# Kernel tuning notes

Measured on AMD Instinct MI355X. Metric: run time of the kernel, lower is better.

Reference implementation:

```python
import jax, jax.numpy as jnp
import numpy as np

NHEAD = 8


def _global_query_attention(cs, ks, vs):
    """cs: (B,H,G,Ek) global queries; ks: (B,H,S,Ek); vs: (B,H,S,Ev).
    For each key position i: v'_i = sum_{s<=i} softmax(K[:i] @ q) * V[:i].
    Returns (B,H,S,G,Ev)."""
    w = jnp.exp(jnp.einsum('bhge,bhse->bhgs', cs, ks))          # (B,H,G,S)
    norms = jnp.cumsum(w, axis=-1)                               # (B,H,G,S)
    wv = w[..., None] * vs[:, :, None, :, :]                     # (B,H,G,S,Ev) -- huge intermediate
    resp = jnp.cumsum(wv, axis=-2) / norms[..., None]            # (B,H,G,S,Ev)
    return jnp.swapaxes(resp, -3, -2)                            # (B,H,S,G,Ev)


def setup_inputs() -> dict:
    B, L, E, G = 4, 2048, 512, 16
    KD = VD = E
    keys = jax.random.split(jax.random.key(0), 9)
    s_qk = 0.02              # keep exp(q.k) finite in fp32
    s_v = 1.0 / np.sqrt(VD).astype(np.float32)
    return {
        'query':        jax.random.normal(keys[0], (B, L, E), jnp.float32),
        'key':          jax.random.normal(keys[1], (B, L, E), jnp.float32),
        'value':        jax.random.normal(keys[2], (B, L, E), jnp.float32),
        'context':      jax.random.normal(keys[3], (B, G, E), jnp.float32),
        'query_proj':   jax.random.normal(keys[4], (1, E, KD), jnp.float32) * s_qk,
        'key_proj':     jax.random.normal(keys[5], (1, E, KD), jnp.float32) * s_qk,
        'value_proj':   jax.random.normal(keys[6], (1, E, VD), jnp.float32) * s_v,
        'output_proj':  jax.random.normal(keys[7], (1, VD, E), jnp.float32) * s_v,
        'context_proj': jax.random.normal(keys[8], (1, E, KD), jnp.float32) * s_qk,
    }


def reference(query, key, value, context, query_proj, key_proj, value_proj, output_proj, context_proj):
    B, L, E = query.shape
    G = context.shape[1]
    H = NHEAD
    KD = query_proj.shape[-1]
    VD = value_proj.shape[-1]
    Ek, Ev = KD // H, VD // H

    def heads(x, W, n, dh):
        # (B,n,E) @ (1,E,D) -> (B,n,D) -> (B,H,n,dh)
        return jnp.swapaxes((x @ W).reshape(B, n, H, dh), 1, 2)

    cs = heads(context, context_proj, G, Ek)   # (B,H,G,Ek)
    qs = heads(query, query_proj, L, Ek)       # (B,H,L,Ek)
    ks = heads(key, key_proj, L, Ek)           # (B,H,S,Ek)
    vs = heads(value, value_proj, L, Ev)       # (B,H,S,Ev)

    resp_v = _global_query_attention(cs, ks, vs)   # (B,H,S,G,Ev)
    resp_k = _global_query_attention(cs, ks, ks)   # (B,H,S,G,Ek)

    logits = jnp.einsum('bhse,bhsge->bhsg', qs, resp_k)   # (B,H,S,G)
    w = jax.nn.softmax(logits, axis=-1)
    out = jnp.einsum('bhsg,bhsge->bhse', w, resp_v)       # (B,H,S,Ev)
    out = jnp.swapaxes(out, 1, 2).reshape(B, L, VD)       # (B,S,vdim)
    return out @ output_proj                               # (B,S,d_model)
```

## Files before the change

### kernel.cpp

```cpp
#include <hip/hip_runtime.h>
#include <hip/hip_bf16.h>

#define NB 4
#define SL 2048
#define NG 16
#define NH 8
#define DH 64
#define NBH (NB * NH)
#define NCH (SL / 64)

typedef __attribute__((ext_vector_type(8))) short bh8;
typedef __attribute__((ext_vector_type(4))) float fx4;

__device__ __forceinline__ ushort f2bf(float x) {
    union { float f; unsigned u; } v; v.f = x;
    const unsigned r = v.u + 0x7fffu + ((v.u >> 16) & 1u);
    return (ushort)(r >> 16);
}
__device__ __forceinline__ float b2f(ushort u) {
    union { unsigned u; float f; } v; v.u = ((unsigned)u) << 16;
    return v.f;
}
__device__ __forceinline__ bh8 pack8(float4 lo, float4 hi) {
    bh8 r;
    r[0] = (short)f2bf(lo.x); r[1] = (short)f2bf(lo.y);
    r[2] = (short)f2bf(lo.z); r[3] = (short)f2bf(lo.w);
    r[4] = (short)f2bf(hi.x); r[5] = (short)f2bf(hi.y);
    r[6] = (short)f2bf(hi.z); r[7] = (short)f2bf(hi.w);
    return r;
}
__device__ __forceinline__ void unpack8(bh8 v, float4& lo, float4& hi) {
    lo.x = b2f((ushort)v[0]); lo.y = b2f((ushort)v[1]);
    lo.z = b2f((ushort)v[2]); lo.w = b2f((ushort)v[3]);
    hi.x = b2f((ushort)v[4]); hi.y = b2f((ushort)v[5]);
    hi.z = b2f((ushort)v[6]); hi.w = b2f((ushort)v[7]);
}

__global__ __launch_bounds__(256) void convT512_4(const float* __restrict__ w0,
                                                  const float* __restrict__ w1,
                                                  const float* __restrict__ w2,
                                                  const float* __restrict__ w3,
                                                  ushort* __restrict__ o0,
                                                  ushort* __restrict__ o1,
                                                  ushort* __restrict__ o2,
                                                  ushort* __restrict__ o3) {
    const int z = blockIdx.z;
    const float* W = (z == 0) ? w0 : (z == 1) ? w1 : (z == 2) ? w2 : w3;
    ushort* WT = (z == 0) ? o0 : (z == 1) ? o1 : (z == 2) ? o2 : o3;
    __shared__ float tile[32][33];
    const int bx = blockIdx.x * 32, by = blockIdx.y * 32;
    const int tx = threadIdx.x & 31, ty = threadIdx.x >> 5;
#pragma unroll
    for (int p = 0; p < 4; ++p)
        tile[ty + p * 8][tx] = W[(size_t)(by + ty + p * 8) * 512 + bx + tx];
    __syncthreads();
#pragma unroll
    for (int p = 0; p < 4; ++p)
        WT[(size_t)(bx + ty + p * 8) * 512 + by + tx] = f2bf(tile[tx][ty + p * 8]);
}

__global__ __launch_bounds__(256, 6) void gemm_qkv_kernel(
    const float* __restrict__ qf, const float* __restrict__ kf,
    const float* __restrict__ vf, const ushort* __restrict__ qpT,
    const ushort* __restrict__ kpT, const ushort* __restrict__ vpT,
    ushort* __restrict__ qsb, ushort* __restrict__ ksb, ushort* __restrict__ vsb) {
    const int z = blockIdx.z;
    const float* A32 = (z == 0) ? qf : (z == 1) ? kf : vf;
    const ushort* BT = (z == 0) ? qpT : (z == 1) ? kpT : vpT;
    ushort* out = (z == 0) ? qsb : (z == 1) ? ksb : vsb;

    __shared__ __align__(16) ushort As[2][64 * 32];
    __shared__ __align__(16) ushort Bs[2][128 * 32];
    const int t = threadIdx.x;
    const int lane = t & 63, w = t >> 6;
    const int bm = blockIdx.x * 64, bn = blockIdx.y * 128;
    const int ea = t * 8;
    const size_t arow = (size_t)(bm + (ea >> 5)) * 512 + (ea & 31);
    const int eb0 = w * 1024 + lane * 8;
    const int eb1 = eb0 + 512;
    const size_t b0 = (size_t)(bn + (eb0 >> 5)) * 512 + (eb0 & 31);
    const size_t b1 = (size_t)(bn + (eb1 >> 5)) * 512 + (eb1 & 31);
    const int wr = w >> 1, wc = w & 1;
    const int fr = lane & 15, kg = lane >> 4;
    const int aoff = (wr * 32 + fr) * 32 + kg * 8;
    const int boff = (wc * 64 + fr) * 32 + kg * 8;
    fx4 acc[2][4] = {};
    float4 a0v, a1v;

#define LOADA(kk)                                                              \
    do {                                                                       \
        a0v = *(const float4*)&A32[arow + (kk)];                               \
        a1v = *(const float4*)&A32[arow + (kk) + 4];                           \
    } while (0)
#define WRITEA(buf) do { *(bh8*)&As[buf][ea] = pack8(a0v, a1v); } while (0)
#define STAGEB(buf, kk)                                                        \
    do {                                                                       \
        __builtin_amdgcn_global_load_lds(                                      \
            (const __attribute__((address_space(1))) void*)(BT + b0 + (kk)),   \
            (__attribute__((address_space(3))) void*)&Bs[buf][w * 1024], 16, 0, 0); \
        __builtin_amdgcn_global_load_lds(                                      \
            (const __attribute__((address_space(1))) void*)(BT + b1 + (kk)),   \
            (__attribute__((address_space(3))) void*)&Bs[buf][w * 1024 + 512], 16, 0, 0); \
    } while (0)

    LOADA(0);
    STAGEB(0, 0);
    WRITEA(0);
    LOADA(32);
    __syncthreads();
    int cur = 0;
    for (int k0 = 0; k0 < 512; k0 += 32) {
        if (k0 + 32 < 512) {
            STAGEB(cur ^ 1, k0 + 32);
            WRITEA(cur ^ 1);
            if (k0 + 64 < 512) LOADA(k0 + 64);
        }
        bh8 af[2], bf[4];
#pragma unroll
        for (int m = 0; m < 2; ++m) af[m] = *(const bh8*)&As[cur][aoff + m * 512];
#pragma unroll
        for (int nn = 0; nn < 4; ++nn) bf[nn] = *(const bh8*)&Bs[cur][boff + nn * 512];
#pragma unroll
        for (int m = 0; m < 2; ++m)
#pragma unroll
            for (int nn = 0; nn < 4; ++nn)
                acc[m][nn] = __builtin_amdgcn_mfma_f32_16x16x32_bf16(
                    af[m], bf[nn], acc[m][nn], 0, 0, 0);
        __syncthreads();
        cur ^= 1;
    }
#undef LOADA
#undef WRITEA
#undef STAGEB
#pragma unroll
    for (int m = 0; m < 2; ++m)
#pragma unroll
        for (int nn = 0; nn < 4; ++nn)
#pragma unroll
            for (int j = 0; j < 4; ++j) {
                const int r = bm + wr * 32 + m * 16 + kg * 4 + j;
                const int cc = bn + wc * 64 + nn * 16 + fr;
                const int b = r >> 11, i = r & 2047;
                out[(((size_t)(b * NH) + (cc >> 6)) * SL + i) * DH + (cc & 63)] =
                    f2bf(acc[m][nn][j]);
            }
}

__global__ __launch_bounds__(256) void gemm_out_kernel(const ushort* __restrict__ A,
                                                       const ushort* __restrict__ BT,
                                                       float* __restrict__ out) {
    __shared__ __align__(16) ushort As[2][64 * 32];
    __shared__ __align__(16) ushort Bs[2][64 * 32];
    const int t = threadIdx.x;
    const int lane = t & 63, w = t >> 6;
    const int bm = blockIdx.x * 64, bn = blockIdx.y * 64;
    const int e0 = w * 512 + lane * 8;
    const size_t a0 = (size_t)(bm + (e0 >> 5)) * 512 + (e0 & 31);
    const size_t b0 = (size_t)(bn + (e0 >> 5)) * 512 + (e0 & 31);
    const int wr = w >> 1, wc = w & 1;
    const int fr = lane & 15, kg = lane >> 4;
    const int aoff = (wr * 32 + fr) * 32 + kg * 8;
    const int boff = (wc * 32 + fr) * 32 + kg * 8;
    fx4 acc[2][2] = {};

#define STAGE_O(buf, kk)                                                           \
    do {                                                                           \
        __builtin_amdgcn_global_load_lds(                                          \
            (const __attribute__((address_space(1))) void*)(A + a0 + (kk)),        \
            (__attribute__((address_space(3))) void*)&As[buf][w * 512], 16, 0, 0); \
        __builtin_amdgcn_global_load_lds(                                          \
            (const __attribute__((address_space(1))) void*)(BT + b0 + (kk)),       \
            (__attribute__((address_space(3))) void*)&Bs[buf][w * 512], 16, 0, 0); \
    } while (0)

    STAGE_O(0, 0);
    __syncthreads();
    int cur = 0;
    for (int k0 = 0; k0 < 512; k0 += 32) {
        if (k0 + 32 < 512) STAGE_O(cur ^ 1, k0 + 32);
        bh8 af[2], bf[2];
#pragma unroll
        for (int m = 0; m < 2; ++m) af[m] = *(const bh8*)&As[cur][aoff + m * 512];
#pragma unroll
        for (int nn = 0; nn < 2; ++nn) bf[nn] = *(const bh8*)&Bs[cur][boff + nn * 512];
#pragma unroll
        for (int m = 0; m < 2; ++m)
#pragma unroll
            for (int nn = 0; nn < 2; ++nn)
                acc[m][nn] = __builtin_amdgcn_mfma_f32_16x16x32_bf16(
                    af[m], bf[nn], acc[m][nn], 0, 0, 0);
        __syncthreads();
        cur ^= 1;
    }
#undef STAGE_O
#pragma unroll
    for (int m = 0; m < 2; ++m)
#pragma unroll
        for (int nn = 0; nn < 2; ++nn)
#pragma unroll
            for (int j = 0; j < 4; ++j) {
                const int r = bm + wr * 32 + m * 16 + kg * 4 + j;
                const int cc = bn + wc * 32 + nn * 16 + fr;
                out[(size_t)r * 512 + cc] = acc[m][nn][j];
            }
}

template <int MODE>
__global__ __launch_bounds__(256) void gemm512(const float* __restrict__ X,
                                               const float* __restrict__ Wm,
                                               float* __restrict__ out, int n) {
    __shared__ float As[16][65];
    __shared__ float Bs[16][64];
    const int t = threadIdx.x;
    const int rm = blockIdx.x * 64;
    const int cn = blockIdx.y * 64;
    const int tm = t >> 4, tn = t & 15;
    const int arow = t >> 2, ak = (t & 3) << 2;
    const int bk = t >> 4, bc = (t & 15) << 2;
    float acc[4][4] = {};
    for (int k0 = 0; k0 < 512; k0 += 16) {
        float4 av = *(const float4*)&X[(size_t)(rm + arow) * 512 + k0 + ak];
        float4 bv = *(const float4*)&Wm[(size_t)(k0 + bk) * 512 + cn + bc];
        __syncthreads();
        As[ak + 0][arow] = av.x;
        As[ak + 1][arow] = av.y;
        As[ak + 2][arow] = av.z;
        As[ak + 3][arow] = av.w;
        *(float4*)&Bs[bk][bc] = bv;
        __syncthreads();
#pragma unroll
        for (int kk = 0; kk < 16; ++kk) {
            float a0 = As[kk][tm * 4 + 0], a1 = As[kk][tm * 4 + 1];
            float a2 = As[kk][tm * 4 + 2], a3 = As[kk][tm * 4 + 3];
            float4 b = *(const float4*)&Bs[kk][tn * 4];
            acc[0][0] += a0 * b.x; acc[0][1] += a0 * b.y; acc[0][2] += a0 * b.z; acc[0][3] += a0 * b.w;
            acc[1][0] += a1 * b.x; acc[1][1] += a1 * b.y; acc[1][2] += a1 * b.z; acc[1][3] += a1 * b.w;
            acc[2][0] += a2 * b.x; acc[2][1] += a2 * b.y; acc[2][2] += a2 * b.z; acc[2][3] += a2 * b.w;
            acc[3][0] += a3 * b.x; acc[3][1] += a3 * b.y; acc[3][2] += a3 * b.z; acc[3][3] += a3 * b.w;
        }
    }
#pragma unroll
    for (int j = 0; j < 4; ++j) {
        const int r = rm + tm * 4 + j;
#pragma unroll
        for (int jj = 0; jj < 4; ++jj) {
            const int cc = cn + tn * 4 + jj;
            if (MODE == 0) {
                const int b = r / n, i = r % n;
                out[(((size_t)(b * NH) + (cc >> 6)) * n + i) * DH + (cc & 63)] = acc[j][jj];
            } else {
                out[(size_t)r * 512 + cc] = acc[j][jj];
            }
        }
    }
}

__global__ __launch_bounds__(256) void chunk_sums_w_kernel(
    const ushort* __restrict__ ksb, const ushort* __restrict__ vsb,
    const float* __restrict__ cs, float* __restrict__ wb,
    float* __restrict__ Mc, float* __restrict__ Nc) {
    const int bh = blockIdx.x, c = blockIdx.y;
    __shared__ float Ks[64 * 64];
    __shared__ float Vs[64 * 64];
    __shared__ float Ws[64 * 16];
    __shared__ float Cs[16][65];
    const int t = threadIdx.x;
    const ushort* kbase = ksb + ((size_t)bh * SL + c * 64) * DH;
    const ushort* vbase = vsb + ((size_t)bh * SL + c * 64) * DH;
#pragma unroll
    for (int p = 0; p < 2; ++p) {
        const int idx = (p * 256 + t) * 8;
        float4 lo, hi;
        unpack8(*(const bh8*)&kbase[idx], lo, hi);
        *(float4*)&Ks[idx] = lo; *(float4*)&Ks[idx + 4] = hi;
        unpack8(*(const bh8*)&vbase[idx], lo, hi);
        *(float4*)&Vs[idx] = lo; *(float4*)&Vs[idx + 4] = hi;
    }
    {
        const int idx = t * 4;
        const float4 cv = *(const float4*)&cs[(size_t)bh * NG * DH + idx];
        const int g = idx >> 6, e = idx & 63;
        Cs[g][e + 0] = cv.x; Cs[g][e + 1] = cv.y; Cs[g][e + 2] = cv.z; Cs[g][e + 3] = cv.w;
    }
    __syncthreads();
    {
        const int i = (t * 4) >> 4, g0 = (t * 4) & 15;
        float d0 = 0.f, d1 = 0.f, d2 = 0.f, d3 = 0.f;
#pragma unroll 8
        for (int e = 0; e < 64; ++e) {
            const float kv = Ks[i * 64 + e];
            d0 += kv * Cs[g0 + 0][e];
            d1 += kv * Cs[g0 + 1][e];
            d2 += kv * Cs[g0 + 2][e];
            d3 += kv * Cs[g0 + 3][e];
        }
        float4 wv;
        wv.x = expf(d0); wv.y = expf(d1); wv.z = expf(d2); wv.w = expf(d3);
        *(float4*)&Ws[i * 16 + g0] = wv;
        *(float4*)&wb[((size_t)bh * SL + c * 64 + i) * NG + g0] = wv;
    }
    __syncthreads();
    const int e = t >> 2, g0 = (t & 3) * 4;
    float m0 = 0.f, m1 = 0.f, m2 = 0.f, m3 = 0.f;
#pragma unroll 8
    for (int i = 0; i < 64; ++i) {
        const float kv = Ks[i * 64 + e];
        const float4 w = *(const float4*)&Ws[i * 16 + g0];
        m0 += kv * w.x; m1 += kv * w.y; m2 += kv * w.z; m3 += kv * w.w;
    }
    const int g2 = t >> 4, e2 = (t & 15) * 4;
    float n0 = 0.f, n1 = 0.f, n2 = 0.f, n3 = 0.f;
#pragma unroll 8
    for (int i = 0; i < 64; ++i) {
        const float wv = Ws[i * 16 + g2];
        const float4 vv = *(const float4*)&Vs[i * 64 + e2];
        n0 += wv * vv.x; n1 += wv * vv.y; n2 += wv * vv.z; n3 += wv * vv.w;
    }
    float* mo = Mc + ((size_t)(bh * NCH + c) * 64 + e) * 16 + g0;
    mo[0] = m0; mo[1] = m1; mo[2] = m2; mo[3] = m3;
    float* no = Nc + ((size_t)(bh * NCH + c) * 16 + g2) * 64 + e2;
    no[0] = n0; no[1] = n1; no[2] = n2; no[3] = n3;
}

__global__ __launch_bounds__(256) void scans_kernel(const float* __restrict__ wb,
                                                    float* __restrict__ nb,
                                                    float* __restrict__ Mc,
                                                    float* __restrict__ Nc) {
    const int bid = blockIdx.x;
    const int t = threadIdx.x;
    if (bid < NBH * NG) {
        const int bh = bid >> 4, g = bid & 15;
        __shared__ float sw[2048];
        __shared__ float sp[256];
        for (int p = 0; p < 8; ++p) {
            const int s = p * 256 + t;
            sw[s] = wb[((size_t)bh * SL + s) * NG + g];
        }
        __syncthreads();
        float loc[8];
        float run = 0.f;
#pragma unroll
        for (int j = 0; j < 8; ++j) { run += sw[t * 8 + j]; loc[j] = run; }
        sp[t] = run;
        __syncthreads();
        for (int off = 1; off < 256; off <<= 1) {
            const float v = sp[t];
            const float add = (t >= off) ? sp[t - off] : 0.f;
            __syncthreads();
            sp[t] = v + add;
            __syncthreads();
        }
        const float offs = (t > 0) ? sp[t - 1] : 0.f;
#pragma unroll
        for (int j = 0; j < 8; ++j)
            nb[(size_t)bid * SL + t * 8 + j] = offs + loc[j];
    } else {
        const int idx = bid - NBH * NG;
        const int bh = idx >> 1;
        float* base = ((idx & 1) ? Nc : Mc) + (size_t)bh * NCH * 1024;
        float4 run = make_float4(0.f, 0.f, 0.f, 0.f);
        float4 nxt = *(float4*)&base[t * 4];
        for (int c = 0; c < NCH; ++c) {
            const float4 v = nxt;
            if (c + 1 < NCH) nxt = *(float4*)&base[(c + 1) * 1024 + t * 4];
            *(float4*)&base[c * 1024 + t * 4] = run;
            run.x += v.x; run.y += v.y; run.z += v.z; run.w += v.w;
        }
    }
}

__global__ __launch_bounds__(256) void pass1c_kernel(const ushort* __restrict__ qsb,
                                                     const ushort* __restrict__ ksb,
                                                     const float* __restrict__ wb,
                                                     const float* __restrict__ nb,
                                                     const float* __restrict__ Mc,
                                                     float* __restrict__ cb) {
    const int bh = blockIdx.x;
    const int r = blockIdx.y;
    const int s0 = r * 64;
    __shared__ float Qs[64][65];
    __shared__ float Kt[64][65];
    __shared__ float At[64][65];
    __shared__ float Wt[64 * 16];
    __shared__ float Pt[64 * 16];
    __shared__ float Lg[64][17];
    const int t = threadIdx.x;
    const int am = t >> 4, an = t & 15;
    const ushort* qbase = qsb + ((size_t)bh * SL + s0) * DH;
    const ushort* kbase = ksb + ((size_t)bh * SL + s0) * DH;
#pragma unroll
    for (int p = 0; p < 2; ++p) {
        const int idx = (p * 256 + t) * 8;
        const int row = idx >> 6, col = idx & 63;
        float4 lo, hi;
        unpack8(*(const bh8*)&qbase[idx], lo, hi);
        *(float4*)&Qs[row][col] = lo; *(float4*)&Qs[row][col + 4] = hi;
        unpack8(*(const bh8*)&kbase[idx], lo, hi);
        *(float4*)&Kt[row][col] = lo; *(float4*)&Kt[row][col + 4] = hi;
    }
    *(float4*)&Wt[t * 4] = *(const float4*)&wb[((size_t)bh * SL + s0) * NG + t * 4];
    *(float4*)&Pt[t * 4] = *(const float4*)&Mc[(size_t)(bh * NCH + r) * 1024 + t * 4];
    __syncthreads();
    float a[4][4] = {};
#pragma unroll 8
    for (int e = 0; e < 64; ++e) {
        float qv[4], kv[4];
#pragma unroll
        for (int j = 0; j < 4; ++j) qv[j] = Qs[am * 4 + j][e];
#pragma unroll
        for (int jj = 0; jj < 4; ++jj) kv[jj] = Kt[an * 4 + jj][e];
#pragma unroll
        for (int j = 0; j < 4; ++j)
#pragma unroll
            for (int jj = 0; jj < 4; ++jj) a[j][jj] += qv[j] * kv[jj];
    }
#pragma unroll
    for (int j = 0; j < 4; ++j)
#pragma unroll
        for (int jj = 0; jj < 4; ++jj) {
            if (an * 4 + jj > am * 4 + j) a[j][jj] = 0.f;
            At[am * 4 + j][an * 4 + jj] = a[j][jj];
        }
    __syncthreads();
    float lg[4] = {0.f, 0.f, 0.f, 0.f};
#pragma unroll 8
    for (int ii = 0; ii < 64; ++ii) {
        const float wv = Wt[ii * 16 + an];
#pragma unroll
        for (int j = 0; j < 4; ++j) lg[j] += At[am * 4 + j][ii] * wv;
    }
#pragma unroll 8
    for (int e = 0; e < 64; ++e) {
        const float pv = Pt[e * 16 + an];
#pragma unroll
        for (int j = 0; j < 4; ++j) lg[j] += Qs[am * 4 + j][e] * pv;
    }
#pragma unroll
    for (int j = 0; j < 4; ++j) Lg[am * 4 + j][an] = lg[j];
    __syncthreads();
    if (t < 64) {
        const int s = s0 + t;
        const float* nbase = nb + (size_t)bh * NG * SL + s;
        float nv[16], l[16];
        float mx = -1e30f;
#pragma unroll
        for (int g = 0; g < 16; ++g) {
            nv[g] = nbase[(size_t)g * SL];
            l[g] = Lg[t][g] / nv[g];
            mx = fmaxf(mx, l[g]);
        }
        float sum = 0.f;
#pragma unroll
        for (int g = 0; g < 16; ++g) { l[g] = expf(l[g] - mx); sum += l[g]; }
        const float inv = 1.f / sum;
#pragma unroll
        for (int g = 0; g < 16; ++g)
            cb[((size_t)bh * SL + s) * NG + g] = l[g] * inv / nv[g];
    }
}

__global__ __launch_bounds__(256) void pass2c_kernel(const float* __restrict__ cb,
                                                     const float* __restrict__ wb,
                                                     const ushort* __restrict__ vsb,
                                                     const float* __restrict__ Nc,
                                                     ushort* __restrict__ ohb) {
    const int bh = blockIdx.x;
    const int b = bh >> 3, h = bh & 7;
    const int r = blockIdx.y;
    const int s0 = r * 64;
    __shared__ float Ct[64][17];
    __shared__ float Wt[64][17];
    __shared__ float Vt[64 * 64];
    __shared__ float St[64][65];
    __shared__ float Ut[16 * 64];
    const int t = threadIdx.x;
    const int am = t >> 4, an = t & 15;
    {
        const int idx = t * 4;
        const int row = idx >> 4, g0 = idx & 15;
        const float4 cv = *(const float4*)&cb[((size_t)bh * SL + s0) * NG + idx];
        Ct[row][g0 + 0] = cv.x; Ct[row][g0 + 1] = cv.y;
        Ct[row][g0 + 2] = cv.z; Ct[row][g0 + 3] = cv.w;
        const float4 wv = *(const float4*)&wb[((size_t)bh * SL + s0) * NG + idx];
        Wt[row][g0 + 0] = wv.x; Wt[row][g0 + 1] = wv.y;
        Wt[row][g0 + 2] = wv.z; Wt[row][g0 + 3] = wv.w;
    }
    const ushort* vbase = vsb + ((size_t)bh * SL + s0) * DH;
#pragma unroll
    for (int p = 0; p < 2; ++p) {
        const int idx = (p * 256 + t) * 8;
        float4 lo, hi;
        unpack8(*(const bh8*)&vbase[idx], lo, hi);
        *(float4*)&Vt[idx] = lo; *(float4*)&Vt[idx + 4] = hi;
    }
    *(float4*)&Ut[t * 4] = *(const float4*)&Nc[(size_t)(bh * NCH + r) * 1024 + t * 4];
    __syncthreads();
    float sv[4][4] = {};
#pragma unroll
    for (int g = 0; g < 16; ++g) {
        float cv[4], wv[4];
#pragma unroll
        for (int j = 0; j < 4; ++j) cv[j] = Ct[am * 4 + j][g];
#pragma unroll
        for (int jj = 0; jj < 4; ++jj) wv[jj] = Wt[an * 4 + jj][g];
#pragma unroll
        for (int j = 0; j < 4; ++j)
#pragma unroll
            for (int jj = 0; jj < 4; ++jj) sv[j][jj] += cv[j] * wv[jj];
    }
#pragma unroll
    for (int j = 0; j < 4; ++j)
#pragma unroll
        for (int jj = 0; jj < 4; ++jj) {
            if (an * 4 + jj > am * 4 + j) sv[j][jj] = 0.f;
            St[am * 4 + j][an * 4 + jj] = sv[j][jj];
        }
    __syncthreads();
    float acc[4][4] = {};
#pragma unroll
    for (int g = 0; g < 16; ++g) {
        const float4 u = *(const float4*)&Ut[g * 64 + an * 4];
        float cv[4];
#pragma unroll
        for (int j = 0; j < 4; ++j) cv[j] = Ct[am * 4 + j][g];
#pragma unroll
        for (int j = 0; j < 4; ++j) {
            acc[j][0] += cv[j] * u.x; acc[j][1] += cv[j] * u.y;
            acc[j][2] += cv[j] * u.z; acc[j][3] += cv[j] * u.w;
        }
    }
#pragma unroll 8
    for (int ii = 0; ii < 64; ++ii) {
        const float4 vv = *(const float4*)&Vt[ii * 64 + an * 4];
        float st[4];
#pragma unroll
        for (int j = 0; j < 4; ++j) st[j] = St[am * 4 + j][ii];
#pragma unroll
        for (int j = 0; j < 4; ++j) {
            acc[j][0] += st[j] * vv.x; acc[j][1] += st[j] * vv.y;
            acc[j][2] += st[j] * vv.z; acc[j][3] += st[j] * vv.w;
        }
    }
#pragma unroll
    for (int j = 0; j < 4; ++j) {
        const int s = s0 + am * 4 + j;
        ushort4 pk;
        pk.x = f2bf(acc[j][0]); pk.y = f2bf(acc[j][1]);
        pk.z = f2bf(acc[j][2]); pk.w = f2bf(acc[j][3]);
        *(ushort4*)&ohb[((size_t)b * SL + s) * 512 + h * DH + an * 4] = pk;
    }
}

extern "C" void kernel_launch(void* const* d_in, const int* in_sizes, int n_in,
                              void* d_out, int out_size, void* d_ws, size_t ws_size,
                              hipStream_t stream) {
    const float* query   = (const float*)d_in[0];
    const float* key     = (const float*)d_in[1];
    const float* value   = (const float*)d_in[2];
    const float* context = (const float*)d_in[3];
    const float* qp = (const float*)d_in[4];
    const float* kp = (const float*)d_in[5];
    const float* vp = (const float*)d_in[6];
    const float* op = (const float*)d_in[7];
    const float* cp = (const float*)d_in[8];
    float* out = (float*)d_out;

    ushort* qsb = (ushort*)d_ws;
    ushort* ksb = qsb + 4194304;
    ushort* vsb = ksb + 4194304;
    ushort* ohb = vsb + 4194304;
    ushort* qpT = ohb + 4194304;
    ushort* kpT = qpT + 262144;
    ushort* vpT = kpT + 262144;
    ushort* opT = vpT + 262144;
    float* fbase = (float*)(opT + 262144);
    float* cs = fbase;
    float* wb = cs + 32768;
    float* nb = wb + 1048576;
    float* Mc = nb + 1048576;
    float* Nc = Mc + 1048576;
    float* cb = Nc + 1048576;

    dim3 blk(256);
    convT512_4<<<dim3(16, 16, 4), blk, 0, stream>>>(qp, kp, vp, op, qpT, kpT, vpT, opT);
    gemm512<0><<<dim3(1, 8), blk, 0, stream>>>(context, cp, cs, NG);
    gemm_qkv_kernel<<<dim3(128, 4, 3), blk, 0, stream>>>(query, key, value,
                                                         qpT, kpT, vpT, qsb, ksb, vsb);
    chunk_sums_w_kernel<<<dim3(NBH, NCH), blk, 0, stream>>>(ksb, vsb, cs, wb, Mc, Nc);
    scans_kernel<<<dim3(NBH * NG + NBH * 2), blk, 0, stream>>>(wb, nb, Mc, Nc);
    pass1c_kernel<<<dim3(NBH, NCH), blk, 0, stream>>>(qsb, ksb, wb, nb, Mc, cb);
    pass2c_kernel<<<dim3(NBH, NCH), blk, 0, stream>>>(cb, wb, vsb, Nc, ohb);
    gemm_out_kernel<<<dim3(128, 8), blk, 0, stream>>>(ohb, opT, out);
}
```

Measured before the change: 152.9 us.

## Widen GEMM K-tiles with XOR-swizzled LDS and transpose weights for coalesced scans

```diff
diff --git a/kernel.cpp b/kernel.cpp
--- a/kernel.cpp
+++ b/kernel.cpp
@@ -34,6 +34,9 @@
     lo.z = b2f((ushort)v[2]); lo.w = b2f((ushort)v[3]);
     hi.x = b2f((ushort)v[4]); hi.y = b2f((ushort)v[5]);
     hi.z = b2f((ushort)v[6]); hi.w = b2f((ushort)v[7]);
+}
+__device__ __forceinline__ int swz(int row, int col) {
+    return row * 64 + (col ^ ((row & 7) << 3));
 }
 
 __global__ __launch_bounds__(256) void convT512_4(const float* __restrict__ w0,
@@ -59,7 +62,7 @@
         WT[(size_t)(bx + ty + p * 8) * 512 + by + tx] = f2bf(tile[tx][ty + p * 8]);
 }
 
-__global__ __launch_bounds__(256, 6) void gemm_qkv_kernel(
+__global__ __launch_bounds__(256, 3) void gemm_qkv_kernel(
     const float* __restrict__ qf, const float* __restrict__ kf,
     const float* __restrict__ vf, const ushort* __restrict__ qpT,
     const ushort* __restrict__ kpT, const ushort* __restrict__ vpT,
@@ -69,63 +72,80 @@
     const ushort* BT = (z == 0) ? qpT : (z == 1) ? kpT : vpT;
     ushort* out = (z == 0) ? qsb : (z == 1) ? ksb : vsb;
 
-    __shared__ __align__(16) ushort As[2][64 * 32];
-    __shared__ __align__(16) ushort Bs[2][128 * 32];
+    __shared__ __align__(16) ushort As[2][64 * 64];
+    __shared__ __align__(16) ushort Bs[2][128 * 64];
     const int t = threadIdx.x;
     const int lane = t & 63, w = t >> 6;
     const int bm = blockIdx.x * 64, bn = blockIdx.y * 128;
-    const int ea = t * 8;
-    const size_t arow = (size_t)(bm + (ea >> 5)) * 512 + (ea & 31);
-    const int eb0 = w * 1024 + lane * 8;
-    const int eb1 = eb0 + 512;
-    const size_t b0 = (size_t)(bn + (eb0 >> 5)) * 512 + (eb0 & 31);
-    const size_t b1 = (size_t)(bn + (eb1 >> 5)) * 512 + (eb1 & 31);
+    const int ar = t >> 2, ao = (t & 3) * 16;
+    const size_t abase = (size_t)(bm + ar) * 512 + ao;
+    const int asw0 = swz(ar, ao), asw1 = swz(ar, ao + 8);
+    size_t bsrc[4];
+#pragma unroll
+    for (int i = 0; i < 4; ++i) {
+        const int s = w * 2048 + i * 512 + lane * 8;
+        const int r = s >> 6, o = (s & 63) ^ ((r & 7) << 3);
+        bsrc[i] = (size_t)(bn + r) * 512 + o;
+    }
     const int wr = w >> 1, wc = w & 1;
     const int fr = lane & 15, kg = lane >> 4;
-    const int aoff = (wr * 32 + fr) * 32 + kg * 8;
-    const int boff = (wc * 64 + fr) * 32 + kg * 8;
     fx4 acc[2][4] = {};
-    float4 a0v, a1v;
+    float4 a0v, a1v, a2v, a3v;
 
 #define LOADA(kk)                                                              \
     do {                                                                       \
-        a0v = *(const float4*)&A32[arow + (kk)];                               \
-        a1v = *(const float4*)&A32[arow + (kk) + 4];                           \
+        a0v = *(const float4*)&A32[abase + (kk)];                              \
+        a1v = *(const float4*)&A32[abase + (kk) + 4];                          \
+        a2v = *(const float4*)&A32[abase + (kk) + 8];                          \
+        a3v = *(const float4*)&A32[abase + (kk) + 12];                         \
     } while (0)
-#define WRITEA(buf) do { *(bh8*)&As[buf][ea] = pack8(a0v, a1v); } while (0)
+#define WRITEA(buf)                                                            \
+    do {                                                                       \
+        *(bh8*)&As[buf][asw0] = pack8(a0v, a1v);                               \
+        *(bh8*)&As[buf][asw1] = pack8(a2v, a3v);                               \
+    } while (0)
 #define STAGEB(buf, kk)                                                        \
     do {                                                                       \
-        __builtin_amdgcn_global_load_lds(                                      \
-            (const __attribute__((address_space(1))) void*)(BT + b0 + (kk)),   \
-            (__attribute__((address_space(3))) void*)&Bs[buf][w * 1024], 16, 0, 0); \
-        __builtin_amdgcn_global_load_lds(                                      \
-            (const __attribute__((address_space(1))) void*)(BT + b1 + (kk)),   \
-            (__attribute__((address_space(3))) void*)&Bs[buf][w * 1024 + 512], 16, 0, 0); \
+        _Pragma("unroll")                                                      \
+        for (int i = 0; i < 4; ++i)                                            \
+            __builtin_amdgcn_global_load_lds(                                  \
+                (const __attribute__((address_space(1))) void*)(BT + bsrc[i] + (kk)), \
+                (__attribute__((address_space(3))) void*)&Bs[buf][w * 2048 + i * 512], \
+                16, 0, 0);                                                     \
     } while (0)
 
     LOADA(0);
     STAGEB(0, 0);
     WRITEA(0);
-    LOADA(32);
+    LOADA(64);
     __syncthreads();
     int cur = 0;
-    for (int k0 = 0; k0 < 512; k0 += 32) {
-        if (k0 + 32 < 512) {
-            STAGEB(cur ^ 1, k0 + 32);
+    for (int k0 = 0; k0 < 512; k0 += 64) {
+        if (k0 + 64 < 512) {
+            STAGEB(cur ^ 1, k0 + 64);
             WRITEA(cur ^ 1);
-            if (k0 + 64 < 512) LOADA(k0 + 64);
-        }
-        bh8 af[2], bf[4];
-#pragma unroll
-        for (int m = 0; m < 2; ++m) af[m] = *(const bh8*)&As[cur][aoff + m * 512];
-#pragma unroll
-        for (int nn = 0; nn < 4; ++nn) bf[nn] = *(const bh8*)&Bs[cur][boff + nn * 512];
-#pragma unroll
-        for (int m = 0; m < 2; ++m)
-#pragma unroll
-            for (int nn = 0; nn < 4; ++nn)
-                acc[m][nn] = __builtin_amdgcn_mfma_f32_16x16x32_bf16(
-                    af[m], bf[nn], acc[m][nn], 0, 0, 0);
+            if (k0 + 128 < 512) LOADA(k0 + 128);
+        }
+#pragma unroll
+        for (int kk = 0; kk < 2; ++kk) {
+            bh8 af[2], bf[4];
+#pragma unroll
+            for (int m = 0; m < 2; ++m) {
+                const int R = wr * 32 + m * 16 + fr;
+                af[m] = *(const bh8*)&As[cur][swz(R, kk * 32 + kg * 8)];
+            }
+#pragma unroll
+            for (int nn = 0; nn < 4; ++nn) {
+                const int C = wc * 64 + nn * 16 + fr;
+                bf[nn] = *(const bh8*)&Bs[cur][swz(C, kk * 32 + kg * 8)];
+            }
+#pragma unroll
+            for (int m = 0; m < 2; ++m)
+#pragma unroll
+                for (int nn = 0; nn < 4; ++nn)
+                    acc[m][nn] = __builtin_amdgcn_mfma_f32_16x16x32_bf16(
+                        af[m], bf[nn], acc[m][nn], 0, 0, 0);
+        }
         __syncthreads();
         cur ^= 1;
     }
@@ -146,49 +166,72 @@
             }
 }
 
-__global__ __launch_bounds__(256) void gemm_out_kernel(const ushort* __restrict__ A,
-                                                       const ushort* __restrict__ BT,
-                                                       float* __restrict__ out) {
-    __shared__ __align__(16) ushort As[2][64 * 32];
-    __shared__ __align__(16) ushort Bs[2][64 * 32];
+__global__ __launch_bounds__(256, 3) void gemm_out_kernel(const ushort* __restrict__ A,
+                                                          const ushort* __restrict__ BT,
+                                                          float* __restrict__ out) {
+    __shared__ __align__(16) ushort As[2][64 * 64];
+    __shared__ __align__(16) ushort Bs[2][128 * 64];
     const int t = threadIdx.x;
     const int lane = t & 63, w = t >> 6;
-    const int bm = blockIdx.x * 64, bn = blockIdx.y * 64;
-    const int e0 = w * 512 + lane * 8;
-    const size_t a0 = (size_t)(bm + (e0 >> 5)) * 512 + (e0 & 31);
-    const size_t b0 = (size_t)(bn + (e0 >> 5)) * 512 + (e0 & 31);
+    const int bm = blockIdx.x * 64, bn = blockIdx.y * 128;
+    size_t asrc[2], bsrc[4];
+#pragma unroll
+    for (int i = 0; i < 2; ++i) {
+        const int s = w * 1024 + i * 512 + lane * 8;
+        const int r = s >> 6, o = (s & 63) ^ ((r & 7) << 3);
+        asrc[i] = (size_t)(bm + r) * 512 + o;
+    }
+#pragma unroll
+    for (int i = 0; i < 4; ++i) {
+        const int s = w * 2048 + i * 512 + lane * 8;
+        const int r = s >> 6, o = (s & 63) ^ ((r & 7) << 3);
+        bsrc[i] = (size_t)(bn + r) * 512 + o;
+    }
     const int wr = w >> 1, wc = w & 1;
     const int fr = lane & 15, kg = lane >> 4;
-    const int aoff = (wr * 32 + fr) * 32 + kg * 8;
-    const int boff = (wc * 32 + fr) * 32 + kg * 8;
-    fx4 acc[2][2] = {};
-
-#define STAGE_O(buf, kk)                                                           \
-    do {                                                                           \
-        __builtin_amdgcn_global_load_lds(                                          \
-            (const __attribute__((address_space(1))) void*)(A + a0 + (kk)),        \
-            (__attribute__((address_space(3))) void*)&As[buf][w * 512], 16, 0, 0); \
-        __builtin_amdgcn_global_load_lds(                                          \
-            (const __attribute__((address_space(1))) void*)(BT + b0 + (kk)),       \
-            (__attribute__((address_space(3))) void*)&Bs[buf][w * 512], 16, 0, 0); \
+    fx4 acc[2][4] = {};
+
+#define STAGE_O(buf, kk)                                                       \
+    do {                                                                       \
+        _Pragma("unroll")                                                      \
+        for (int i = 0; i < 2; ++i)                                            \
+            __builtin_amdgcn_global_load_lds(                                  \
+                (const __attribute__((address_space(1))) void*)(A + asrc[i] + (kk)), \
+                (__attribute__((address_space(3))) void*)&As[buf][w * 1024 + i * 512], \
+                16, 0, 0);                                                     \
+        _Pragma("unroll")                                                      \
+        for (int i = 0; i < 4; ++i)                                            \
+            __builtin_amdgcn_global_load_lds(                                  \
+                (const __attribute__((address_space(1))) void*)(BT + bsrc[i] + (kk)), \
+                (__attribute__((address_space(3))) void*)&Bs[buf][w * 2048 + i * 512], \
+                16, 0, 0);                                                     \
     } while (0)
 
     STAGE_O(0, 0);
     __syncthreads();
     int cur = 0;
-    for (int k0 = 0; k0 < 512; k0 += 32) {
-        if (k0 + 32 < 512) STAGE_O(cur ^ 1, k0 + 32);
-        bh8 af[2], bf[2];
-#pragma unroll
-        for (int m = 0; m < 2; ++m) af[m] = *(const bh8*)&As[cur][aoff + m * 512];
-#pragma unroll
-        for (int nn = 0; nn < 2; ++nn) bf[nn] = *(const bh8*)&Bs[cur][boff + nn * 512];
-#pragma unroll
-        for (int m = 0; m < 2; ++m)
-#pragma unroll
-            for (int nn = 0; nn < 2; ++nn)
-                acc[m][nn] = __builtin_amdgcn_mfma_f32_16x16x32_bf16(
-                    af[m], bf[nn], acc[m][nn], 0, 0, 0);
+    for (int k0 = 0; k0 < 512; k0 += 64) {
+        if (k0 + 64 < 512) STAGE_O(cur ^ 1, k0 + 64);
+#pragma unroll
+        for (int kk = 0; kk < 2; ++kk) {
+            bh8 af[2], bf[4];
+#pragma unroll
+            for (int m = 0; m < 2; ++m) {
+                const int R = wr * 32 + m * 16 + fr;
+                af[m] = *(const bh8*)&As[cur][swz(R, kk * 32 + kg * 8)];
+            }
+#pragma unroll
+            for (int nn = 0; nn < 4; ++nn) {
+                const int C = wc * 64 + nn * 16 + fr;
+                bf[nn] = *(const bh8*)&Bs[cur][swz(C, kk * 32 + kg * 8)];
+            }
+#pragma unroll
+            for (int m = 0; m < 2; ++m)
+#pragma unroll
+                for (int nn = 0; nn < 4; ++nn)
+                    acc[m][nn] = __builtin_amdgcn_mfma_f32_16x16x32_bf16(
+                        af[m], bf[nn], acc[m][nn], 0, 0, 0);
+        }
         __syncthreads();
         cur ^= 1;
     }
@@ -196,11 +239,11 @@
 #pragma unroll
     for (int m = 0; m < 2; ++m)
 #pragma unroll
-        for (int nn = 0; nn < 2; ++nn)
+        for (int nn = 0; nn < 4; ++nn)
 #pragma unroll
             for (int j = 0; j < 4; ++j) {
                 const int r = bm + wr * 32 + m * 16 + kg * 4 + j;
-                const int cc = bn + wc * 32 + nn * 16 + fr;
+                const int cc = bn + wc * 64 + nn * 16 + fr;
                 out[(size_t)r * 512 + cc] = acc[m][nn][j];
             }
 }
@@ -258,7 +301,7 @@
 __global__ __launch_bounds__(256) void chunk_sums_w_kernel(
     const ushort* __restrict__ ksb, const ushort* __restrict__ vsb,
     const float* __restrict__ cs, float* __restrict__ wb,
-    float* __restrict__ Mc, float* __restrict__ Nc) {
+    float* __restrict__ wbT, float* __restrict__ Mc, float* __restrict__ Nc) {
     const int bh = blockIdx.x, c = blockIdx.y;
     __shared__ float Ks[64 * 64];
     __shared__ float Vs[64 * 64];
@@ -300,6 +343,15 @@
         *(float4*)&wb[((size_t)bh * SL + c * 64 + i) * NG + g0] = wv;
     }
     __syncthreads();
+    {
+        const int g = t >> 4, i0 = (t & 15) * 4;
+        float4 wv4;
+        wv4.x = Ws[(i0 + 0) * 16 + g];
+        wv4.y = Ws[(i0 + 1) * 16 + g];
+        wv4.z = Ws[(i0 + 2) * 16 + g];
+        wv4.w = Ws[(i0 + 3) * 16 + g];
+        *(float4*)&wbT[((size_t)(bh * NG) + g) * SL + c * 64 + i0] = wv4;
+    }
     const int e = t >> 2, g0 = (t & 3) * 4;
     float m0 = 0.f, m1 = 0.f, m2 = 0.f, m3 = 0.f;
 #pragma unroll 8
@@ -322,19 +374,19 @@
     no[0] = n0; no[1] = n1; no[2] = n2; no[3] = n3;
 }
 
-__global__ __launch_bounds__(256) void scans_kernel(const float* __restrict__ wb,
+__global__ __launch_bounds__(256) void scans_kernel(const float* __restrict__ wbT,
                                                     float* __restrict__ nb,
                                                     float* __restrict__ Mc,
                                                     float* __restrict__ Nc) {
     const int bid = blockIdx.x;
     const int t = threadIdx.x;
     if (bid < NBH * NG) {
-        const int bh = bid >> 4, g = bid & 15;
         __shared__ float sw[2048];
         __shared__ float sp[256];
-        for (int p = 0; p < 8; ++p) {
-            const int s = p * 256 + t;
-            sw[s] = wb[((size_t)bh * SL + s) * NG + g];
+#pragma unroll
+        for (int p = 0; p < 2; ++p) {
+            const int idx = (p * 256 + t) * 4;
+            *(float4*)&sw[idx] = *(const float4*)&wbT[(size_t)bid * SL + idx];
         }
         __syncthreads();
         float loc[8];
@@ -580,15 +632,16 @@
     float* Mc = nb + 1048576;
     float* Nc = Mc + 1048576;
     float* cb = Nc + 1048576;
+    float* wbT = cb + 1048576;
 
     dim3 blk(256);
     convT512_4<<<dim3(16, 16, 4), blk, 0, stream>>>(qp, kp, vp, op, qpT, kpT, vpT, opT);
     gemm512<0><<<dim3(1, 8), blk, 0, stream>>>(context, cp, cs, NG);
     gemm_qkv_kernel<<<dim3(128, 4, 3), blk, 0, stream>>>(query, key, value,
                                                          qpT, kpT, vpT, qsb, ksb, vsb);
-    chunk_sums_w_kernel<<<dim3(NBH, NCH), blk, 0, stream>>>(ksb, vsb, cs, wb, Mc, Nc);
-    scans_kernel<<<dim3(NBH * NG + NBH * 2), blk, 0, stream>>>(wb, nb, Mc, Nc);
+    chunk_sums_w_kernel<<<dim3(NBH, NCH), blk, 0, stream>>>(ksb, vsb, cs, wb, wbT, Mc, Nc);
+    scans_kernel<<<dim3(NBH * NG + NBH * 2), blk, 0, stream>>>(wbT, nb, Mc, Nc);
     pass1c_kernel<<<dim3(NBH, NCH), blk, 0, stream>>>(qsb, ksb, wb, nb, Mc, cb);
     pass2c_kernel<<<dim3(NBH, NCH), blk, 0, stream>>>(cb, wb, vsb, Nc, ohb);
-    gemm_out_kernel<<<dim3(128, 8), blk, 0, stream>>>(ohb, opT, out);
-}
+    gemm_out_kernel<<<dim3(128, 4), blk, 0, stream>>>(ohb, opT, out);
+}
```

Measured after the change: 150.3 us. Within noise of the previous version (-1.7%).
